# Performance work log

Hardware: AMD Instinct MI355X
Metric: run time of the kernel (lower is better)

The kernel has to match this reference:

```python
import jax, jax.numpy as jnp
import numpy as np

B, S, D = 2, 1024, 2048
H, HKV, HD = 16, 4, 128


def _rotate_half(x):
    x1, x2 = jnp.split(x, 2, axis=-1)
    return jnp.concatenate([-x2, x1], axis=-1)


def setup_inputs() -> dict:
    key = jax.random.key(0)
    ks = jax.random.split(key, 8)
    hidden_states = jax.random.normal(ks[0], (B, S, D), dtype=jnp.float32)
    position_ids = jnp.tile(jnp.arange(S, dtype=jnp.int32)[None, :], (B, 1))
    active_mask = jax.random.bernoulli(ks[1], 0.5, (B, S))
    active_mask = active_mask.at[:, 0].set(True)  # ensure >=1 causal valid key per query
    # standard RoPE tables
    inv_freq = 1.0 / (10000.0 ** (jnp.arange(0, HD, 2, dtype=jnp.float32) / HD))
    freqs = jnp.arange(S, dtype=jnp.float32)[:, None] * inv_freq[None, :]
    emb = jnp.concatenate([freqs, freqs], axis=-1)  # [S, HD]
    cos, sin = jnp.cos(emb), jnp.sin(emb)
    scale = 0.02
    wq = jax.random.normal(ks[2], (D, H * HD), dtype=jnp.float32) * scale
    wk = jax.random.normal(ks[3], (D, HKV * HD), dtype=jnp.float32) * scale
    wv = jax.random.normal(ks[4], (D, HKV * HD), dtype=jnp.float32) * scale
    wo = jax.random.normal(ks[5], (H * HD, D), dtype=jnp.float32) * scale
    return {"hidden_states": hidden_states, "cos": cos, "sin": sin,
            "wq": wq, "wk": wk, "wv": wv, "wo": wo,
            "position_ids": position_ids, "active_mask": active_mask}


def reference(hidden_states, cos, sin, wq, wk, wv, wo, position_ids, active_mask):
    b, s, d = hidden_states.shape
    groups = H // HKV
    scale = HD ** -0.5

    q = (hidden_states @ wq).reshape(b, s, H, HD).transpose(0, 2, 1, 3)    # [b,H,s,hd]
    k = (hidden_states @ wk).reshape(b, s, HKV, HD).transpose(0, 2, 1, 3)  # [b,Hkv,s,hd]
    v = (hidden_states @ wv).reshape(b, s, HKV, HD).transpose(0, 2, 1, 3)

    cs, sn = cos[None, None], sin[None, None]  # [1,1,s,hd]
    q = q * cs + _rotate_half(q) * sn
    k = k * cs + _rotate_half(k) * sn

    # SelectiveKVCache.update_selective (prefill from empty cache):
    # per-batch gather of active tokens, padded (k/v with 0, positions with -1).
    # Padding to full s is math-equivalent to padding to max_active (padded
    # slots are masked with -inf below).
    ar = jnp.arange(s, dtype=jnp.int32)
    order = jnp.argsort(jnp.where(active_mask, ar, ar + s), axis=1)        # actives first, stable order
    sorted_mask = jnp.take_along_axis(active_mask, order, axis=1)          # [b,s]
    gidx = order[:, None, :, None]
    k_sel = jnp.take_along_axis(k, gidx, axis=2) * sorted_mask[:, None, :, None]
    v_sel = jnp.take_along_axis(v, gidx, axis=2) * sorted_mask[:, None, :, None]
    pos_sel = jnp.where(sorted_mask, jnp.take_along_axis(position_ids, order, axis=1), -1)  # [b,s]

    # GQA: repeat kv heads
    k_rep = jnp.repeat(k_sel, groups, axis=1)  # [b,H,skv,hd]
    v_rep = jnp.repeat(v_sel, groups, axis=1)

    scores = jnp.einsum('bhqd,bhkd->bhqk', q, k_rep) * scale
    valid = (pos_sel >= 0)[:, None, None, :]                               # [b,1,1,skv]
    causal = (pos_sel[:, None, :] <= position_ids[:, :, None])[:, None]    # [b,1,q,skv]
    big_neg = jnp.finfo(scores.dtype).min
    scores = jnp.where(valid & causal, scores, big_neg)

    attn = jax.nn.softmax(scores, axis=-1)
    out = jnp.einsum('bhqk,bhkd->bhqd', attn, v_rep)
    out = out.transpose(0, 2, 1, 3).reshape(b, s, H * HD)
    return out @ wo
```

## Files before the change

### kernel.cpp

```cpp
#include <hip/hip_runtime.h>
#include <hip/hip_bf16.h>

#define Bn 2
#define Sn 1024
#define Dn 2048
#define Hn 16
#define HKVn 4
#define HDn 128

typedef __attribute__((ext_vector_type(8))) short s8v;
typedef __attribute__((ext_vector_type(8))) unsigned short u8v;
typedef __attribute__((ext_vector_type(4))) float f4v;
typedef __hip_bfloat16 bf16;

typedef __attribute__((address_space(3))) void lds_void;
typedef __attribute__((address_space(1))) const void gbl_void;
#define ASYNC_LD16(g, l) \
  __builtin_amdgcn_global_load_lds((gbl_void*)(g), (lds_void*)(l), 16, 0, 0)

static __device__ __forceinline__ unsigned short f2b_bits(float f) {
  bf16 h = __float2bfloat16(f);
  return __builtin_bit_cast(unsigned short, h);
}

__global__ void mask_norm(const void* __restrict__ mraw, unsigned char* __restrict__ m8, int n) {
  __shared__ int bytemode;
  if (threadIdx.x == 0) bytemode = 0;
  __syncthreads();
  const unsigned int* mi = (const unsigned int*)mraw;
  int local = 0;
  for (int t = threadIdx.x; t < n / 4; t += blockDim.x)
    if (mi[t] > 1u) local = 1;
  if (local) atomicOr(&bytemode, 1);
  __syncthreads();
  const int bm = bytemode;
  const unsigned char* mb = (const unsigned char*)mraw;
  for (int t = threadIdx.x; t < n; t += blockDim.x)
    m8[t] = bm ? (mb[t] ? 1 : 0) : (mi[t] != 0u ? 1 : 0);
}

__global__ void cvt_bf16(const float* __restrict__ src, bf16* __restrict__ dst, int n8) {
  int stride = gridDim.x * blockDim.x;
  for (int i = blockIdx.x * blockDim.x + threadIdx.x; i < n8; i += stride) {
    float4 a = reinterpret_cast<const float4*>(src)[2 * i];
    float4 b = reinterpret_cast<const float4*>(src)[2 * i + 1];
    u8v o;
    o[0] = f2b_bits(a.x); o[1] = f2b_bits(a.y); o[2] = f2b_bits(a.z); o[3] = f2b_bits(a.w);
    o[4] = f2b_bits(b.x); o[5] = f2b_bits(b.y); o[6] = f2b_bits(b.z); o[7] = f2b_bits(b.w);
    reinterpret_cast<u8v*>(dst)[i] = o;
  }
}

__global__ __launch_bounds__(256) void transpose_all(
    const float* __restrict__ s0, const float* __restrict__ s1,
    const float* __restrict__ s2, const float* __restrict__ s3,
    bf16* __restrict__ d0, bf16* __restrict__ d1, bf16* __restrict__ d2, bf16* __restrict__ d3) {
  __shared__ float tile[64][65];
  const int z = blockIdx.z;
  const float* src = (z == 0) ? s0 : (z == 1) ? s1 : (z == 2) ? s2 : s3;
  bf16* dst = (z == 0) ? d0 : (z == 1) ? d1 : (z == 2) ? d2 : d3;
  const int N = (z == 1 || z == 2) ? 512 : 2048;
  const int K = Dn;
  const int bx = blockIdx.x * 64;
  if (bx >= N) return;
  const int by = blockIdx.y * 64;
  const int t = threadIdx.x;
  const int lr = t >> 4, lc4 = (t & 15) * 4;
  #pragma unroll
  for (int it = 0; it < 4; ++it) {
    int k = it * 16 + lr;
    float4 v = *reinterpret_cast<const float4*>(&src[(size_t)(by + k) * N + bx + lc4]);
    tile[k][lc4] = v.x; tile[k][lc4 + 1] = v.y; tile[k][lc4 + 2] = v.z; tile[k][lc4 + 3] = v.w;
  }
  __syncthreads();
  #pragma unroll
  for (int it = 0; it < 4; ++it) {
    int n = it * 16 + lr;
    ushort4 o;
    o.x = f2b_bits(tile[lc4 + 0][n]);
    o.y = f2b_bits(tile[lc4 + 1][n]);
    o.z = f2b_bits(tile[lc4 + 2][n]);
    o.w = f2b_bits(tile[lc4 + 3][n]);
    *reinterpret_cast<ushort4*>(&dst[(size_t)(bx + n) * K + by + lc4]) = o;
  }
}

template <int EPI>
__global__ __launch_bounds__(256) void gemm_nt(
    const bf16* __restrict__ A, const bf16* __restrict__ Bt,
    bf16* __restrict__ Oq, bf16* __restrict__ Ok, bf16* __restrict__ Ov,
    float* __restrict__ Of, int K, int N) {
  __shared__ __align__(16) bf16 Al[128 * 64];
  __shared__ __align__(16) bf16 Bl[128 * 64];
  const int tid = threadIdx.x;
  const int lane = tid & 63, w = tid >> 6;
  const int wm = (w >> 1) * 64, wn = (w & 1) * 64;
  const int m0 = blockIdx.y * 128, n0 = blockIdx.x * 128;
  const int l16 = lane & 15, lg = lane >> 4;
  const int srow = lane >> 3;
  const int sch = lane & 7;
  f4v acc[4][4] = {};
  for (int k0 = 0; k0 < K; k0 += 64) {
    #pragma unroll
    for (int i = 0; i < 4; ++i) {
      const int rb = w * 32 + i * 8;
      const int r = rb + srow;
      const int cs = (sch ^ (r & 7)) * 8;
      ASYNC_LD16(&A[(size_t)(m0 + r) * K + k0 + cs], &Al[rb * 64]);
      ASYNC_LD16(&Bt[(size_t)(n0 + r) * K + k0 + cs], &Bl[rb * 64]);
    }
    __syncthreads();
    #pragma unroll
    for (int kc = 0; kc < 2; ++kc) {
      s8v af[4], bfr[4];
      #pragma unroll
      for (int mf = 0; mf < 4; ++mf) {
        int r = wm + mf * 16 + l16;
        af[mf] = *reinterpret_cast<const s8v*>(&Al[r * 64 + (((kc * 4 + lg) ^ (r & 7)) * 8)]);
      }
      #pragma unroll
      for (int nf = 0; nf < 4; ++nf) {
        int r = wn + nf * 16 + l16;
        bfr[nf] = *reinterpret_cast<const s8v*>(&Bl[r * 64 + (((kc * 4 + lg) ^ (r & 7)) * 8)]);
      }
      #pragma unroll
      for (int mf = 0; mf < 4; ++mf)
        #pragma unroll
        for (int nf = 0; nf < 4; ++nf)
          acc[mf][nf] = __builtin_amdgcn_mfma_f32_16x16x32_bf16(af[mf], bfr[nf], acc[mf][nf], 0, 0, 0);
    }
    __syncthreads();
  }
  #pragma unroll
  for (int mf = 0; mf < 4; ++mf) {
    #pragma unroll
    for (int nf = 0; nf < 4; ++nf) {
      #pragma unroll
      for (int i = 0; i < 4; ++i) {
        int gm = m0 + wm + mf * 16 + lg * 4 + i;
        int gn = n0 + wn + nf * 16 + l16;
        float v = acc[mf][nf][i];
        if (EPI == 0) {
          int b = gm >> 10, s = gm & 1023;
          if (gn < 2048) {
            int h = gn >> 7, hd = gn & 127;
            Oq[(((size_t)(b * Hn + h)) * Sn + s) * HDn + hd] = __float2bfloat16(v);
          } else if (gn < 2560) {
            int t = gn - 2048, kvh = t >> 7, hd = t & 127;
            Ok[(((size_t)(b * HKVn + kvh)) * Sn + s) * HDn + hd] = __float2bfloat16(v);
          } else {
            int t = gn - 2560, kvh = t >> 7, hd = t & 127;
            Ov[(((size_t)(b * HKVn + kvh)) * HDn + hd) * Sn + s] = __float2bfloat16(v);
          }
        } else {
          Of[(size_t)gm * N + gn] = v;
        }
      }
    }
  }
}

__global__ void rope_qk(bf16* __restrict__ qb, bf16* __restrict__ kb,
                        const float* __restrict__ cosp, const float* __restrict__ sinp) {
  const int NQ = Bn * Hn * Sn * 16;
  const int NT = NQ + Bn * HKVn * Sn * 16;
  int stride = gridDim.x * blockDim.x;
  for (int idx = blockIdx.x * blockDim.x + threadIdx.x; idx < NT; idx += stride) {
    bf16* base;
    int rel;
    if (idx < NQ) { base = qb; rel = idx; }
    else          { base = kb; rel = idx - NQ; }
    int d4 = (rel & 15) * 4;
    int s = (rel >> 4) & 1023;
    int head = rel >> 14;
    bf16* p = base + ((size_t)head * Sn + s) * HDn + d4;
    ushort4 a = *reinterpret_cast<ushort4*>(p);
    ushort4 b = *reinterpret_cast<ushort4*>(p + 64);
    float4 c = *reinterpret_cast<const float4*>(&cosp[s * HDn + d4]);
    float4 sv = *reinterpret_cast<const float4*>(&sinp[s * HDn + d4]);
    float x1[4] = {__bfloat162float(__builtin_bit_cast(bf16, a.x)), __bfloat162float(__builtin_bit_cast(bf16, a.y)),
                   __bfloat162float(__builtin_bit_cast(bf16, a.z)), __bfloat162float(__builtin_bit_cast(bf16, a.w))};
    float x2[4] = {__bfloat162float(__builtin_bit_cast(bf16, b.x)), __bfloat162float(__builtin_bit_cast(bf16, b.y)),
                   __bfloat162float(__builtin_bit_cast(bf16, b.z)), __bfloat162float(__builtin_bit_cast(bf16, b.w))};
    float cc[4] = {c.x, c.y, c.z, c.w};
    float ss[4] = {sv.x, sv.y, sv.z, sv.w};
    ushort4 o1, o2;
    unsigned short* o1p = &o1.x; unsigned short* o2p = &o2.x;
    #pragma unroll
    for (int j = 0; j < 4; ++j) {
      o1p[j] = f2b_bits(x1[j] * cc[j] - x2[j] * ss[j]);
      o2p[j] = f2b_bits(x2[j] * cc[j] + x1[j] * ss[j]);
    }
    *reinterpret_cast<ushort4*>(p) = o1;
    *reinterpret_cast<ushort4*>(p + 64) = o2;
  }
}

__global__ __launch_bounds__(256) void attn_fwd(
    const bf16* __restrict__ q, const bf16* __restrict__ k, const bf16* __restrict__ vT,
    const unsigned char* __restrict__ m8, bf16* __restrict__ out) {
  __shared__ __align__(16) bf16 Kl[2][64 * 128];
  __shared__ __align__(16) bf16 Vl[2][128 * 64];
  __shared__ __align__(16) bf16 Pl[4][16 * 72];
  const int tid = threadIdx.x;
  const int lane = tid & 63, w = tid >> 6;
  const int l16 = lane & 15, lg = lane >> 4;
  const int qx = blockIdx.x, h = blockIdx.y, b = blockIdx.z;
  const int NQT = Sn / 64;
  const int qt = (b == 1) ? (NQT - 1 - qx) : qx;
  const int hkv = h >> 2;
  const int q0 = qt * 64 + w * 16;
  const float sl2 = 0.08838834764831845f * 1.44269504088896f;

  const bf16* qp = q + ((size_t)(b * Hn + h) * Sn + q0) * HDn;
  const bf16* kp = k + (size_t)(b * HKVn + hkv) * Sn * HDn;
  const bf16* vp = vT + (size_t)(b * HKVn + hkv) * HDn * Sn;
  const unsigned char* mp = m8 + b * Sn;

  auto stage = [&](int buf, int kbase) {
    #pragma unroll
    for (int i = 0; i < 4; ++i) {
      int ci = i * 256 + w * 64 + lane;
      int kr = ci >> 4, kch = ci & 15;
      ASYNC_LD16(kp + (size_t)(kbase + kr) * HDn + ((kch ^ (kr & 7)) * 8),
                 &Kl[buf][(i * 256 + w * 64) * 8]);
      int vr = ci >> 3, vch = ci & 7;
      ASYNC_LD16(vp + (size_t)vr * Sn + kbase + ((vch ^ (vr & 7)) * 8),
                 &Vl[buf][(i * 256 + w * 64) * 8]);
    }
  };

  s8v qf[4];
  #pragma unroll
  for (int hc = 0; hc < 4; ++hc)
    qf[hc] = *reinterpret_cast<const s8v*>(qp + l16 * HDn + hc * 32 + lg * 8);

  float mrow[4], lrow[4];
  f4v o[8] = {};
  #pragma unroll
  for (int i = 0; i < 4; ++i) { mrow[i] = -1e30f; lrow[i] = 0.f; }

  stage(0, 0);
  __syncthreads();

  for (int kt = 0; kt <= qt; ++kt) {
    const int cur = kt & 1;
    const int kb = kt * 64;
    if (kt < qt) stage(cur ^ 1, kb + 64);

    f4v sc[4] = {};
    #pragma unroll
    for (int ktc = 0; ktc < 4; ++ktc) {
      #pragma unroll
      for (int hc = 0; hc < 4; ++hc) {
        int r = ktc * 16 + l16;
        s8v kf = *reinterpret_cast<const s8v*>(
            &Kl[cur][r * 128 + (((hc * 4 + lg) ^ (r & 7)) * 8)]);
        sc[ktc] = __builtin_amdgcn_mfma_f32_16x16x32_bf16(qf[hc], kf, sc[ktc], 0, 0, 0);
      }
    }
    float pm[4];
    #pragma unroll
    for (int i = 0; i < 4; ++i) pm[i] = -1e30f;
    int act[4];
    #pragma unroll
    for (int ktc = 0; ktc < 4; ++ktc) act[ktc] = mp[kb + ktc * 16 + l16];
    if (kt == qt) {
      #pragma unroll
      for (int ktc = 0; ktc < 4; ++ktc) {
        int j = kb + ktc * 16 + l16;
        #pragma unroll
        for (int i = 0; i < 4; ++i) {
          int qr = q0 + lg * 4 + i;
          float v = sc[ktc][i] * sl2;
          v = (act[ktc] && j <= qr) ? v : -1e30f;
          sc[ktc][i] = v;
          pm[i] = fmaxf(pm[i], v);
        }
      }
    } else {
      #pragma unroll
      for (int ktc = 0; ktc < 4; ++ktc) {
        #pragma unroll
        for (int i = 0; i < 4; ++i) {
          float v = sc[ktc][i] * sl2;
          v = act[ktc] ? v : -1e30f;
          sc[ktc][i] = v;
          pm[i] = fmaxf(pm[i], v);
        }
      }
    }
    #pragma unroll
    for (int off = 1; off < 16; off <<= 1)
      #pragma unroll
      for (int i = 0; i < 4; ++i) pm[i] = fmaxf(pm[i], __shfl_xor(pm[i], off, 64));
    float fac[4];
    #pragma unroll
    for (int i = 0; i < 4; ++i) {
      float mn = fmaxf(mrow[i], pm[i]);
      fac[i] = exp2f(mrow[i] - mn);
      mrow[i] = mn;
    }
    float rs[4] = {0.f, 0.f, 0.f, 0.f};
    #pragma unroll
    for (int ktc = 0; ktc < 4; ++ktc)
      #pragma unroll
      for (int i = 0; i < 4; ++i) {
        float p = exp2f(sc[ktc][i] - mrow[i]);
        rs[i] += p;
        Pl[w][(lg * 4 + i) * 72 + ktc * 16 + l16] = __float2bfloat16(p);
      }
    #pragma unroll
    for (int off = 1; off < 16; off <<= 1)
      #pragma unroll
      for (int i = 0; i < 4; ++i) rs[i] += __shfl_xor(rs[i], off, 64);
    #pragma unroll
    for (int i = 0; i < 4; ++i) lrow[i] = lrow[i] * fac[i] + rs[i];
    #pragma unroll
    for (int fn = 0; fn < 8; ++fn)
      #pragma unroll
      for (int i = 0; i < 4; ++i) o[fn][i] *= fac[i];
    #pragma unroll
    for (int kc = 0; kc < 2; ++kc) {
      s8v pf = *reinterpret_cast<const s8v*>(&Pl[w][l16 * 72 + kc * 32 + lg * 8]);
      #pragma unroll
      for (int fn = 0; fn < 8; ++fn) {
        int d = fn * 16 + l16;
        s8v vf = *reinterpret_cast<const s8v*>(
            &Vl[cur][d * 64 + (((kc * 4 + lg) ^ (d & 7)) * 8)]);
        o[fn] = __builtin_amdgcn_mfma_f32_16x16x32_bf16(pf, vf, o[fn], 0, 0, 0);
      }
    }
    __syncthreads();
  }
  #pragma unroll
  for (int fn = 0; fn < 8; ++fn)
    #pragma unroll
    for (int i = 0; i < 4; ++i) {
      int qr = q0 + lg * 4 + i;
      out[((size_t)b * Sn + qr) * (Hn * HDn) + h * HDn + fn * 16 + l16] =
          __float2bfloat16(o[fn][i] / lrow[i]);
    }
}

extern "C" void kernel_launch(void* const* d_in, const int* in_sizes, int n_in,
                              void* d_out, int out_size, void* d_ws, size_t ws_size,
                              hipStream_t stream) {
  const float* hs   = (const float*)d_in[0];
  const float* cosp = (const float*)d_in[1];
  const float* sinp = (const float*)d_in[2];
  const float* wq   = (const float*)d_in[3];
  const float* wk   = (const float*)d_in[4];
  const float* wv   = (const float*)d_in[5];
  const float* wo   = (const float*)d_in[6];
  const void*  am   = d_in[8];

  char* ws = (char*)d_ws;
  bf16* WT  = (bf16*)(ws);
  bf16* woT = (bf16*)(ws + 12582912);
  bf16* qb  = (bf16*)(ws + 12582912 + 8388608);
  bf16* kb  = (bf16*)(ws + 12582912 + 16777216);
  bf16* vT  = (bf16*)(ws + 12582912 + 18874368);
  bf16* ao  = (bf16*)(ws + 12582912 + 20971520);
  unsigned char* m8 = (unsigned char*)(ws + 12582912 + 29360128);
  bf16* hsb = (bf16*)d_out;
  float* outp = (float*)d_out;

  mask_norm<<<1, 256, 0, stream>>>(am, m8, Bn * Sn);
  cvt_bf16<<<2048, 256, 0, stream>>>(hs, hsb, (Bn * Sn * Dn) / 8);
  transpose_all<<<dim3(32, 32, 4), 256, 0, stream>>>(
      wq, wk, wv, wo, WT, WT + (size_t)2048 * Dn, WT + (size_t)2560 * Dn, woT);
  gemm_nt<0><<<dim3(24, 16), 256, 0, stream>>>(hsb, WT, qb, kb, vT, nullptr, Dn, 3072);
  rope_qk<<<1024, 256, 0, stream>>>(qb, kb, cosp, sinp);
  attn_fwd<<<dim3(Sn / 64, Hn, Bn), 256, 0, stream>>>(qb, kb, vT, m8, ao);
  gemm_nt<1><<<dim3(16, 16), 256, 0, stream>>>(ao, woT, nullptr, nullptr, nullptr, outp, Hn * HDn, Dn);
}
```

Before: 246.8 us.

## Double-buffer GEMM LDS tiles and swizzle workgroup order across XCDs

The GEMM kernel now keeps two LDS buffers for A and B. It issues the async global-to-LDS load of the next K tile before computing the MFMAs on the current tile, so memory latency overlaps with math. The launch is also flattened to a 1D grid whose block index is remapped, so consecutive tiles land on the same XCD for better L2 reuse. The cost is double the LDS per workgroup, which may lower occupancy.

```diff
diff --git a/kernel.cpp b/kernel.cpp
--- a/kernel.cpp
+++ b/kernel.cpp
@@ -89,39 +89,51 @@
 __global__ __launch_bounds__(256) void gemm_nt(
     const bf16* __restrict__ A, const bf16* __restrict__ Bt,
     bf16* __restrict__ Oq, bf16* __restrict__ Ok, bf16* __restrict__ Ov,
-    float* __restrict__ Of, int K, int N) {
-  __shared__ __align__(16) bf16 Al[128 * 64];
-  __shared__ __align__(16) bf16 Bl[128 * 64];
+    float* __restrict__ Of, int K, int N, int nbx) {
+  __shared__ __align__(16) bf16 Al[2][128 * 64];
+  __shared__ __align__(16) bf16 Bl[2][128 * 64];
   const int tid = threadIdx.x;
   const int lane = tid & 63, w = tid >> 6;
   const int wm = (w >> 1) * 64, wn = (w & 1) * 64;
-  const int m0 = blockIdx.y * 128, n0 = blockIdx.x * 128;
+  const int nwg = gridDim.x;
+  const int flat = blockIdx.x;
+  const int swz = (flat & 7) * (nwg >> 3) + (flat >> 3);
+  const int m0 = (swz / nbx) * 128, n0 = (swz % nbx) * 128;
   const int l16 = lane & 15, lg = lane >> 4;
   const int srow = lane >> 3;
   const int sch = lane & 7;
   f4v acc[4][4] = {};
-  for (int k0 = 0; k0 < K; k0 += 64) {
+  const int nt = K >> 6;
+
+  auto stage = [&](int buf, int k0) {
     #pragma unroll
     for (int i = 0; i < 4; ++i) {
       const int rb = w * 32 + i * 8;
       const int r = rb + srow;
       const int cs = (sch ^ (r & 7)) * 8;
-      ASYNC_LD16(&A[(size_t)(m0 + r) * K + k0 + cs], &Al[rb * 64]);
-      ASYNC_LD16(&Bt[(size_t)(n0 + r) * K + k0 + cs], &Bl[rb * 64]);
-    }
-    __syncthreads();
+      ASYNC_LD16(&A[(size_t)(m0 + r) * K + k0 + cs], &Al[buf][rb * 64]);
+      ASYNC_LD16(&Bt[(size_t)(n0 + r) * K + k0 + cs], &Bl[buf][rb * 64]);
+    }
+  };
+
+  stage(0, 0);
+  __syncthreads();
+
+  for (int t = 0; t < nt; ++t) {
+    const int cur = t & 1;
+    if (t + 1 < nt) stage(cur ^ 1, (t + 1) << 6);
     #pragma unroll
     for (int kc = 0; kc < 2; ++kc) {
       s8v af[4], bfr[4];
       #pragma unroll
       for (int mf = 0; mf < 4; ++mf) {
         int r = wm + mf * 16 + l16;
-        af[mf] = *reinterpret_cast<const s8v*>(&Al[r * 64 + (((kc * 4 + lg) ^ (r & 7)) * 8)]);
+        af[mf] = *reinterpret_cast<const s8v*>(&Al[cur][r * 64 + (((kc * 4 + lg) ^ (r & 7)) * 8)]);
       }
       #pragma unroll
       for (int nf = 0; nf < 4; ++nf) {
         int r = wn + nf * 16 + l16;
-        bfr[nf] = *reinterpret_cast<const s8v*>(&Bl[r * 64 + (((kc * 4 + lg) ^ (r & 7)) * 8)]);
+        bfr[nf] = *reinterpret_cast<const s8v*>(&Bl[cur][r * 64 + (((kc * 4 + lg) ^ (r & 7)) * 8)]);
       }
       #pragma unroll
       for (int mf = 0; mf < 4; ++mf)
@@ -146,10 +158,10 @@
             int h = gn >> 7, hd = gn & 127;
             Oq[(((size_t)(b * Hn + h)) * Sn + s) * HDn + hd] = __float2bfloat16(v);
           } else if (gn < 2560) {
-            int t = gn - 2048, kvh = t >> 7, hd = t & 127;
+            int t2 = gn - 2048, kvh = t2 >> 7, hd = t2 & 127;
             Ok[(((size_t)(b * HKVn + kvh)) * Sn + s) * HDn + hd] = __float2bfloat16(v);
           } else {
-            int t = gn - 2560, kvh = t >> 7, hd = t & 127;
+            int t2 = gn - 2560, kvh = t2 >> 7, hd = t2 & 127;
             Ov[(((size_t)(b * HKVn + kvh)) * HDn + hd) * Sn + s] = __float2bfloat16(v);
           }
         } else {
@@ -370,8 +382,8 @@
   cvt_bf16<<<2048, 256, 0, stream>>>(hs, hsb, (Bn * Sn * Dn) / 8);
   transpose_all<<<dim3(32, 32, 4), 256, 0, stream>>>(
       wq, wk, wv, wo, WT, WT + (size_t)2048 * Dn, WT + (size_t)2560 * Dn, woT);
-  gemm_nt<0><<<dim3(24, 16), 256, 0, stream>>>(hsb, WT, qb, kb, vT, nullptr, Dn, 3072);
+  gemm_nt<0><<<384, 256, 0, stream>>>(hsb, WT, qb, kb, vT, nullptr, Dn, 3072, 24);
   rope_qk<<<1024, 256, 0, stream>>>(qb, kb, cosp, sinp);
   attn_fwd<<<dim3(Sn / 64, Hn, Bn), 256, 0, stream>>>(qb, kb, vT, m8, ao);
-  gemm_nt<1><<<dim3(16, 16), 256, 0, stream>>>(ao, woT, nullptr, nullptr, nullptr, outp, Hn * HDn, Dn);
-}
+  gemm_nt<1><<<256, 256, 0, stream>>>(ao, woT, nullptr, nullptr, nullptr, outp, Hn * HDn, Dn, 16);
+}
```

Result: faster. 238.1 us (-3.5%).
